# Kernel optimization log

Hardware: AMD Instinct MI355X
Metric: run time of the kernel (lower is better)

## Reference

```python
import jax, jax.numpy as jnp
import numpy as np

NDIR = 6      # build_tree.num_directions()
IDIM = 256
ODIM = 512
B, L, NCH = 8, 4096, 8192


def setup_inputs() -> dict:
    key = jax.random.key(0)
    ks = jax.random.split(key, 9)
    last = jax.random.normal(ks[0], (B, NCH, IDIM), dtype=jnp.float32)
    child_l = jax.random.randint(ks[1], (L,), 0, NCH, dtype=jnp.int32)
    child_r = jax.random.randint(ks[2], (L,), 0, NCH, dtype=jnp.int32)
    vec = jax.random.randint(ks[3], (B, L), 0, NCH, dtype=jnp.int32)
    drev = jax.random.randint(ks[4], (NCH,), 0, 2, dtype=jnp.int32)
    dmap = jax.random.randint(ks[5], (NCH,), 0, NDIR, dtype=jnp.int32)
    # merge FC params: ndir independent Linear(2*idim -> odim) + PReLU(init=relu_weight)
    scale = 1.0 / np.sqrt(2 * IDIM)
    W_merge = jax.random.uniform(ks[6], (NDIR, ODIM, 2 * IDIM), jnp.float32, -scale, scale)
    b_merge = jax.random.uniform(ks[7], (NDIR, ODIM), jnp.float32, -scale, scale)
    alpha_merge = jnp.full((NDIR,), 0.005, dtype=jnp.float32)  # PReLU weight (relu_weight)
    return {"last": last, "W_merge": W_merge, "b_merge": b_merge,
            "alpha_merge": alpha_merge, "child_l": child_l, "child_r": child_r,
            "vec": vec, "drev": drev, "dmap": dmap}


def reference(last, W_merge, b_merge, alpha_merge, child_l, child_r, vec, drev, dmap):
    # child gathers: [B, L, idim]
    lch = last[:, child_l]
    rch = last[:, child_r]
    # per-element direction-reverse blending
    d = drev[vec][:, :, None].astype(last.dtype)          # [B, L, 1]
    a = lch * (1.0 - d) + rch * d
    b = rch * (1.0 - d) + lch * d
    ans = jnp.concatenate([a, b], axis=-1)                # [B, L, 2*idim]
    # routed merge: compute all ndir linears, then select per element (ndir is small)
    y_all = jnp.einsum('bli,doi->bldo', ans, W_merge) + b_merge   # [B, L, ndir, odim]
    dir_idx = dmap[vec]                                   # [B, L] in [0, ndir)
    y = jnp.take_along_axis(y_all, dir_idx[:, :, None, None], axis=2)[:, :, 0]  # [B, L, odim]
    alpha = alpha_merge[dir_idx][:, :, None]              # per-element PReLU slope
    return jnp.where(y > 0, y, alpha * y)
```

## Files before the change

### kernel.cpp

```cpp
#include <hip/hip_runtime.h>
#include <hip/hip_bf16.h>

#define BB 8
#define LL 4096
#define NCH 8192
#define IDIM 256
#define KDIM 512
#define ODIM 512
#define NDIR 6
#define TOT (BB * LL)
#define MT 128

typedef short short8 __attribute__((ext_vector_type(8)));
typedef float floatx4 __attribute__((ext_vector_type(4)));

#define IDX_OFF 64
#define ROWS_OFF (64 + NDIR * TOT)
#define LASTBF_OFF (64 + 2 * NDIR * TOT)
#define LAST_ELEMS (BB * NCH * IDIM)
#define W_ELEMS (NDIR * ODIM * KDIM)
#define N_LAST8 (LAST_ELEMS / 8)
#define N_W8 (W_ELEMS / 8)
#define SCAT_BLK (TOT / 256)
#define CVTL_BLK (N_LAST8 / 256)
#define CVTW_BLK (N_W8 / 256)

__device__ inline void async_copy16(const void* g, void* l) {
  __builtin_amdgcn_global_load_lds(
      (const __attribute__((address_space(1))) void*)g,
      (__attribute__((address_space(3))) void*)l, 16, 0, 0);
}

__device__ inline void cvt8(const float* __restrict__ src,
                            __hip_bfloat16* __restrict__ dst, int i) {
  const floatx4* s = (const floatx4*)src;
  floatx4 a = s[2 * i];
  floatx4 b = s[2 * i + 1];
  union { short8 v; __hip_bfloat16 h[8]; } u;
  u.h[0] = __float2bfloat16(a[0]); u.h[1] = __float2bfloat16(a[1]);
  u.h[2] = __float2bfloat16(a[2]); u.h[3] = __float2bfloat16(a[3]);
  u.h[4] = __float2bfloat16(b[0]); u.h[5] = __float2bfloat16(b[1]);
  u.h[6] = __float2bfloat16(b[2]); u.h[7] = __float2bfloat16(b[3]);
  ((short8*)dst)[i] = u.v;
}

__global__ __launch_bounds__(256) void prep_kernel(
    const int* __restrict__ vec, const int* __restrict__ child_l,
    const int* __restrict__ child_r, const int* __restrict__ drev,
    const int* __restrict__ dmap, const float* __restrict__ last,
    const float* __restrict__ W, int* __restrict__ ws) {
  __hip_bfloat16* last_bf = (__hip_bfloat16*)(ws + LASTBF_OFF);
  __hip_bfloat16* W_bf = last_bf + LAST_ELEMS;
  int bid = blockIdx.x;
  int tid = threadIdx.x;
  if (bid < SCAT_BLK) {
    __shared__ int lcnt[8];
    __shared__ int gbase[8];
    if (tid < 8) lcnt[tid] = 0;
    __syncthreads();
    int t = bid * 256 + tid;
    int l = t & (LL - 1);
    int v = vec[t];
    int dir = dmap[v] & 7;
    int sw = drev[v];
    int cl = child_l[l];
    int cr = child_r[l];
    int r0 = sw ? cr : cl;
    int r1 = sw ? cl : cr;
    int pos = atomicAdd(&lcnt[dir], 1);
    __syncthreads();
    if (tid < 8) gbase[tid] = lcnt[tid] ? atomicAdd(&ws[tid], lcnt[tid]) : 0;
    __syncthreads();
    int slot = dir * TOT + gbase[dir] + pos;
    ws[IDX_OFF + slot] = t;
    ws[ROWS_OFF + slot] = r0 | (r1 << 16);
  } else if (bid < SCAT_BLK + CVTL_BLK) {
    cvt8(last, last_bf, (bid - SCAT_BLK) * 256 + tid);
  } else {
    cvt8(W, W_bf, (bid - SCAT_BLK - CVTL_BLK) * 256 + tid);
  }
}

__global__ __launch_bounds__(256, 2) void gemm_kernel(
    const float* __restrict__ bias, const float* __restrict__ alpha_m,
    const int* __restrict__ ws, float* __restrict__ out) {
  __shared__ __hip_bfloat16 Als[2][128 * 64];
  __shared__ __hip_bfloat16 Bls[2][128 * 64];

  const int mt = blockIdx.y;
  const int nt = blockIdx.x;
  int d = -1, count = 0, m_base = 0;
  {
    int tb = 0;
    for (int dd = 0; dd < NDIR; ++dd) {
      int c = ws[dd];
      int ntile = (c + MT - 1) / MT;
      if (mt < tb + ntile) { d = dd; count = c; m_base = (mt - tb) * MT; break; }
      tb += ntile;
    }
  }
  if (d < 0) return;

  const __hip_bfloat16* last_bf = (const __hip_bfloat16*)(ws + LASTBF_OFF);
  const __hip_bfloat16* W_bf = last_bf + LAST_ELEMS;
  const int* idx = ws + IDX_OFF + d * TOT;
  const int* rows = ws + ROWS_OFF + d * TOT;

  const int tid = threadIdx.x;
  const int wave = __builtin_amdgcn_readfirstlane(tid >> 6);
  const int lane = tid & 63;
  const int lane15 = lane & 15;
  const int quad = lane >> 4;
  const int wm = wave >> 1;
  const int wn = wave & 1;
  const int n_blk = nt * 128;

  const __hip_bfloat16* ap0[4];
  const __hip_bfloat16* ap1[4];
  const __hip_bfloat16* bp[4];
  int ldsrow[4];
#pragma unroll
  for (int i = 0; i < 4; ++i) {
    int sr = wave * 32 + i * 8 + (lane >> 3);
    ldsrow[i] = (wave * 32 + i * 8) * 64;
    int lr = m_base + sr;
    if (lr >= count) lr = count - 1;
    int t = idx[lr] & (TOT - 1);
    int rr = rows[lr];
    int b = t >> 12;
    int r0 = rr & (NCH - 1);
    int r1 = (rr >> 16) & (NCH - 1);
    int xu = ((lane & 7) ^ (sr & 7)) * 8;
    ap0[i] = last_bf + (long long)(b * NCH + r0) * IDIM + xu;
    ap1[i] = last_bf + (long long)(b * NCH + r1) * IDIM + xu;
    bp[i] = W_bf + (long long)(d * ODIM + n_blk + sr) * KDIM + xu;
  }

  floatx4 acc[4][4] = {};
  const int lx = lane15 & 7;

#pragma unroll
  for (int i = 0; i < 4; ++i) {
    async_copy16(ap0[i], &Als[0][ldsrow[i]]);
    async_copy16(bp[i], &Bls[0][ldsrow[i]]);
  }

#pragma unroll
  for (int kt = 0; kt < 8; ++kt) {
    __syncthreads();
    if (kt < 7) {
      const int kn = kt + 1;
      const int nb = kn & 1;
      const int ko = (kn & 3) * 64;
#pragma unroll
      for (int i = 0; i < 4; ++i) {
        const __hip_bfloat16* ga = (kn < 4 ? ap0[i] : ap1[i]) + ko;
        async_copy16(ga, &Als[nb][ldsrow[i]]);
        async_copy16(bp[i] + kn * 64, &Bls[nb][ldsrow[i]]);
      }
    }
    const int c = kt & 1;
#pragma unroll
    for (int s = 0; s < 2; ++s) {
      const int xcol = ((quad + 4 * s) ^ lx) * 8;
      short8 a[4], b[4];
#pragma unroll
      for (int i = 0; i < 4; ++i)
        a[i] = *(const short8*)&Als[c][(wm * 64 + i * 16 + lane15) * 64 + xcol];
#pragma unroll
      for (int j = 0; j < 4; ++j)
        b[j] = *(const short8*)&Bls[c][(wn * 64 + j * 16 + lane15) * 64 + xcol];
#pragma unroll
      for (int i = 0; i < 4; ++i)
#pragma unroll
        for (int j = 0; j < 4; ++j)
          acc[i][j] = __builtin_amdgcn_mfma_f32_16x16x32_bf16(a[i], b[j], acc[i][j], 0, 0, 0);
    }
  }

  const float alpha = alpha_m[d];
  float bj[4];
#pragma unroll
  for (int j = 0; j < 4; ++j)
    bj[j] = bias[d * ODIM + n_blk + wn * 64 + j * 16 + lane15];

#pragma unroll
  for (int i = 0; i < 4; ++i) {
#pragma unroll
    for (int reg = 0; reg < 4; ++reg) {
      int row_id = m_base + wm * 64 + i * 16 + quad * 4 + reg;
      if (row_id >= count) continue;
      int t = idx[row_id] & (TOT - 1);
      float* orow = out + (long long)t * ODIM + n_blk + wn * 64;
#pragma unroll
      for (int j = 0; j < 4; ++j) {
        float y = acc[i][j][reg] + bj[j];
        y = y > 0.f ? y : alpha * y;
        orow[j * 16 + lane15] = y;
      }
    }
  }
}

extern "C" void kernel_launch(void* const* d_in, const int* in_sizes, int n_in,
                              void* d_out, int out_size, void* d_ws, size_t ws_size,
                              hipStream_t stream) {
  const float* last = (const float*)d_in[0];
  const float* W = (const float*)d_in[1];
  const float* bias = (const float*)d_in[2];
  const float* alpha = (const float*)d_in[3];
  const int* child_l = (const int*)d_in[4];
  const int* child_r = (const int*)d_in[5];
  const int* vec = (const int*)d_in[6];
  const int* drev = (const int*)d_in[7];
  const int* dmap = (const int*)d_in[8];

  int* ws = (int*)d_ws;

  hipMemsetAsync(ws, 0, 32, stream);
  prep_kernel<<<SCAT_BLK + CVTL_BLK + CVTW_BLK, 256, 0, stream>>>(
      vec, child_l, child_r, drev, dmap, last, W, ws);
  dim3 grid(ODIM / 128, TOT / MT + NDIR, 1);
  gemm_kernel<<<grid, 256, 0, stream>>>(bias, alpha, ws, (float*)d_out);
}
```

Baseline: 173.9 us.

## Gather fp32 activations directly in GEMM and convert to bf16 in registers

Drops the prepass that converted the whole `last` tensor (64 MB fp32) to bf16. The GEMM now async-copies fp32 rows of `last` into LDS and converts them to bf16 while reading the MFMA fragments. This saves a full read and write of the activation tensor, but doubles the bytes per gathered A tile, raises LDS traffic and conversion ALU work inside the GEMM loop, and replaces double buffering with a single buffer synchronized twice per k-step, so loads no longer overlap compute. The launch bound drops from two blocks per CU to one.

```diff
diff --git a/kernel.cpp b/kernel.cpp
--- a/kernel.cpp
+++ b/kernel.cpp
@@ -16,13 +16,10 @@
 
 #define IDX_OFF 64
 #define ROWS_OFF (64 + NDIR * TOT)
-#define LASTBF_OFF (64 + 2 * NDIR * TOT)
-#define LAST_ELEMS (BB * NCH * IDIM)
+#define WBF_OFF (64 + 2 * NDIR * TOT)
 #define W_ELEMS (NDIR * ODIM * KDIM)
-#define N_LAST8 (LAST_ELEMS / 8)
 #define N_W8 (W_ELEMS / 8)
 #define SCAT_BLK (TOT / 256)
-#define CVTL_BLK (N_LAST8 / 256)
 #define CVTW_BLK (N_W8 / 256)
 
 __device__ inline void async_copy16(const void* g, void* l) {
@@ -31,26 +28,11 @@
       (__attribute__((address_space(3))) void*)l, 16, 0, 0);
 }
 
-__device__ inline void cvt8(const float* __restrict__ src,
-                            __hip_bfloat16* __restrict__ dst, int i) {
-  const floatx4* s = (const floatx4*)src;
-  floatx4 a = s[2 * i];
-  floatx4 b = s[2 * i + 1];
-  union { short8 v; __hip_bfloat16 h[8]; } u;
-  u.h[0] = __float2bfloat16(a[0]); u.h[1] = __float2bfloat16(a[1]);
-  u.h[2] = __float2bfloat16(a[2]); u.h[3] = __float2bfloat16(a[3]);
-  u.h[4] = __float2bfloat16(b[0]); u.h[5] = __float2bfloat16(b[1]);
-  u.h[6] = __float2bfloat16(b[2]); u.h[7] = __float2bfloat16(b[3]);
-  ((short8*)dst)[i] = u.v;
-}
-
 __global__ __launch_bounds__(256) void prep_kernel(
     const int* __restrict__ vec, const int* __restrict__ child_l,
     const int* __restrict__ child_r, const int* __restrict__ drev,
-    const int* __restrict__ dmap, const float* __restrict__ last,
-    const float* __restrict__ W, int* __restrict__ ws) {
-  __hip_bfloat16* last_bf = (__hip_bfloat16*)(ws + LASTBF_OFF);
-  __hip_bfloat16* W_bf = last_bf + LAST_ELEMS;
+    const int* __restrict__ dmap, const float* __restrict__ W,
+    int* __restrict__ ws) {
   int bid = blockIdx.x;
   int tid = threadIdx.x;
   if (bid < SCAT_BLK) {
@@ -74,18 +56,27 @@
     int slot = dir * TOT + gbase[dir] + pos;
     ws[IDX_OFF + slot] = t;
     ws[ROWS_OFF + slot] = r0 | (r1 << 16);
-  } else if (bid < SCAT_BLK + CVTL_BLK) {
-    cvt8(last, last_bf, (bid - SCAT_BLK) * 256 + tid);
   } else {
-    cvt8(W, W_bf, (bid - SCAT_BLK - CVTL_BLK) * 256 + tid);
-  }
-}
-
-__global__ __launch_bounds__(256, 2) void gemm_kernel(
-    const float* __restrict__ bias, const float* __restrict__ alpha_m,
-    const int* __restrict__ ws, float* __restrict__ out) {
-  __shared__ __hip_bfloat16 Als[2][128 * 64];
-  __shared__ __hip_bfloat16 Bls[2][128 * 64];
+    int gid = (bid - SCAT_BLK) * 256 + tid;
+    __hip_bfloat16* W_bf = (__hip_bfloat16*)(ws + WBF_OFF);
+    const floatx4* s = (const floatx4*)W;
+    floatx4 a = s[2 * gid];
+    floatx4 b = s[2 * gid + 1];
+    union { short8 v; __hip_bfloat16 h[8]; } u;
+    u.h[0] = __float2bfloat16(a[0]); u.h[1] = __float2bfloat16(a[1]);
+    u.h[2] = __float2bfloat16(a[2]); u.h[3] = __float2bfloat16(a[3]);
+    u.h[4] = __float2bfloat16(b[0]); u.h[5] = __float2bfloat16(b[1]);
+    u.h[6] = __float2bfloat16(b[2]); u.h[7] = __float2bfloat16(b[3]);
+    ((short8*)W_bf)[gid] = u.v;
+  }
+}
+
+__global__ __launch_bounds__(256) void gemm_kernel(
+    const float* __restrict__ last, const float* __restrict__ bias,
+    const float* __restrict__ alpha_m, const int* __restrict__ ws,
+    float* __restrict__ out) {
+  __shared__ float Als[128 * 64];
+  __shared__ __hip_bfloat16 Bls[128 * 64];
 
   const int mt = blockIdx.y;
   const int nt = blockIdx.x;
@@ -101,8 +92,7 @@
   }
   if (d < 0) return;
 
-  const __hip_bfloat16* last_bf = (const __hip_bfloat16*)(ws + LASTBF_OFF);
-  const __hip_bfloat16* W_bf = last_bf + LAST_ELEMS;
+  const __hip_bfloat16* W_bf = (const __hip_bfloat16*)(ws + WBF_OFF);
   const int* idx = ws + IDX_OFF + d * TOT;
   const int* rows = ws + ROWS_OFF + d * TOT;
 
@@ -115,14 +105,11 @@
   const int wn = wave & 1;
   const int n_blk = nt * 128;
 
-  const __hip_bfloat16* ap0[4];
-  const __hip_bfloat16* ap1[4];
-  const __hip_bfloat16* bp[4];
-  int ldsrow[4];
-#pragma unroll
-  for (int i = 0; i < 4; ++i) {
-    int sr = wave * 32 + i * 8 + (lane >> 3);
-    ldsrow[i] = (wave * 32 + i * 8) * 64;
+  int aoff0[8], aoff1[8], aldsbase[8];
+#pragma unroll
+  for (int i = 0; i < 8; ++i) {
+    int sr = wave * 32 + i * 4 + (lane >> 4);
+    aldsbase[i] = (wave * 32 + i * 4) * 64;
     int lr = m_base + sr;
     if (lr >= count) lr = count - 1;
     int t = idx[lr] & (TOT - 1);
@@ -130,46 +117,61 @@
     int b = t >> 12;
     int r0 = rr & (NCH - 1);
     int r1 = (rr >> 16) & (NCH - 1);
+    int su = ((lane & 15) ^ (sr & 15)) * 4;
+    aoff0[i] = (b * NCH + r0) * IDIM + su;
+    aoff1[i] = (b * NCH + r1) * IDIM + su;
+  }
+  const __hip_bfloat16* bp[4];
+  int bldsbase[4];
+#pragma unroll
+  for (int i = 0; i < 4; ++i) {
+    int sr = wave * 32 + i * 8 + (lane >> 3);
+    bldsbase[i] = (wave * 32 + i * 8) * 64;
     int xu = ((lane & 7) ^ (sr & 7)) * 8;
-    ap0[i] = last_bf + (long long)(b * NCH + r0) * IDIM + xu;
-    ap1[i] = last_bf + (long long)(b * NCH + r1) * IDIM + xu;
     bp[i] = W_bf + (long long)(d * ODIM + n_blk + sr) * KDIM + xu;
   }
 
   floatx4 acc[4][4] = {};
+  const int rx = lane15;
   const int lx = lane15 & 7;
 
 #pragma unroll
-  for (int i = 0; i < 4; ++i) {
-    async_copy16(ap0[i], &Als[0][ldsrow[i]]);
-    async_copy16(bp[i], &Bls[0][ldsrow[i]]);
-  }
-
-#pragma unroll
   for (int kt = 0; kt < 8; ++kt) {
     __syncthreads();
-    if (kt < 7) {
-      const int kn = kt + 1;
-      const int nb = kn & 1;
-      const int ko = (kn & 3) * 64;
+    {
+      const int ko = (kt & 3) * 64;
+      const float* abase = last + ko;
+#pragma unroll
+      for (int i = 0; i < 8; ++i) {
+        const float* ga = abase + (kt < 4 ? aoff0[i] : aoff1[i]);
+        async_copy16(ga, &Als[aldsbase[i]]);
+      }
+#pragma unroll
+      for (int i = 0; i < 4; ++i)
+        async_copy16(bp[i] + kt * 64, &Bls[bldsbase[i]]);
+    }
+    __syncthreads();
+
+#pragma unroll
+    for (int s = 0; s < 2; ++s) {
+      short8 a[4], b[4];
 #pragma unroll
       for (int i = 0; i < 4; ++i) {
-        const __hip_bfloat16* ga = (kn < 4 ? ap0[i] : ap1[i]) + ko;
-        async_copy16(ga, &Als[nb][ldsrow[i]]);
-        async_copy16(bp[i] + kn * 64, &Bls[nb][ldsrow[i]]);
+        const int arow = (wm * 64 + i * 16 + lane15) * 64;
+        const int u0 = s * 8 + quad * 2;
+        floatx4 f0 = *(const floatx4*)&Als[arow + ((u0 ^ rx) * 4)];
+        floatx4 f1 = *(const floatx4*)&Als[arow + (((u0 + 1) ^ rx) * 4)];
+        union { short8 v; __hip_bfloat16 h[8]; } u;
+        u.h[0] = __float2bfloat16(f0[0]); u.h[1] = __float2bfloat16(f0[1]);
+        u.h[2] = __float2bfloat16(f0[2]); u.h[3] = __float2bfloat16(f0[3]);
+        u.h[4] = __float2bfloat16(f1[0]); u.h[5] = __float2bfloat16(f1[1]);
+        u.h[6] = __float2bfloat16(f1[2]); u.h[7] = __float2bfloat16(f1[3]);
+        a[i] = u.v;
       }
-    }
-    const int c = kt & 1;
-#pragma unroll
-    for (int s = 0; s < 2; ++s) {
       const int xcol = ((quad + 4 * s) ^ lx) * 8;
-      short8 a[4], b[4];
-#pragma unroll
-      for (int i = 0; i < 4; ++i)
-        a[i] = *(const short8*)&Als[c][(wm * 64 + i * 16 + lane15) * 64 + xcol];
 #pragma unroll
       for (int j = 0; j < 4; ++j)
-        b[j] = *(const short8*)&Bls[c][(wn * 64 + j * 16 + lane15) * 64 + xcol];
+        b[j] = *(const short8*)&Bls[(wn * 64 + j * 16 + lane15) * 64 + xcol];
 #pragma unroll
       for (int i = 0; i < 4; ++i)
 #pragma unroll
@@ -218,8 +220,8 @@
   int* ws = (int*)d_ws;
 
   hipMemsetAsync(ws, 0, 32, stream);
-  prep_kernel<<<SCAT_BLK + CVTL_BLK + CVTW_BLK, 256, 0, stream>>>(
-      vec, child_l, child_r, drev, dmap, last, W, ws);
+  prep_kernel<<<SCAT_BLK + CVTW_BLK, 256, 0, stream>>>(
+      vec, child_l, child_r, drev, dmap, W, ws);
   dim3 grid(ODIM / 128, TOT / MT + NDIR, 1);
-  gemm_kernel<<<grid, 256, 0, stream>>>(bias, alpha, ws, (float*)d_out);
-}
+  gemm_kernel<<<grid, 256, 0, stream>>>(last, bias, alpha, ws, (float*)d_out);
+}
```

Result: slower. 180.5 us (+3.8%).
